# Kernel optimization log

Hardware: AMD Instinct MI355X
Metric: run time of the kernel (lower is better)

## Reference

```python
import jax, jax.numpy as jnp
import numpy as np

EMBED_DIM = 2048
NUM_HEADS = 16
HEAD_DIM = EMBED_DIM // NUM_HEADS  # 128
D_K = 128
SCALE = 1.0 / float(np.sqrt(HEAD_DIM))
LAYER_DEPTH = 6 / 12  # amrpa_layer_idx / n_amrpa_layers
BATCH, SEQ = 2, 2048


def setup_inputs() -> dict:
    key = jax.random.key(0)
    ks = jax.random.split(key, 8)
    return {
        "hidden_states": jax.random.normal(ks[0], (BATCH, SEQ, EMBED_DIM), jnp.float32),
        "c_attn_w": jax.random.normal(ks[1], (EMBED_DIM, 3 * EMBED_DIM), jnp.float32) * 0.02,
        "c_attn_b": jax.random.normal(ks[2], (3 * EMBED_DIM,), jnp.float32) * 0.02,
        "c_proj_w": jax.random.normal(ks[3], (EMBED_DIM, EMBED_DIM), jnp.float32) * 0.02,
        "c_proj_b": jax.random.normal(ks[4], (EMBED_DIM,), jnp.float32) * 0.02,
        "cam_gate": jax.random.normal(ks[5], (D_K,), jnp.float32) * 0.1,
        "cam_w0": jax.random.normal(ks[6], (1,), jnp.float32),
        "cam_w1": jax.random.normal(ks[7], (1,), jnp.float32),
    }


def reference(hidden_states, c_attn_w, c_attn_b, c_proj_w, c_proj_b, cam_gate, cam_w0, cam_w1):
    # GPT2 Conv1D-style fused QKV projection: [B,S,3E]
    qkv = hidden_states @ c_attn_w + c_attn_b
    Q, K, V = jnp.split(qkv, 3, axis=2)  # each [B,S,E]
    # NOTE: faithful to source — attention over the FULL embed dim (no head split),
    # scaled by 1/sqrt(head_dim); causal mask is computed but never applied upstream.
    attn_scores = jnp.einsum('bse,bte->bst', Q, K) * SCALE  # [B,S,S]

    # CAM: sliced low-rank channels
    Q_cam, K_cam, V_cam = Q[:, :, :D_K], K[:, :, :D_K], V[:, :, :D_K]
    # base attention map computed under no_grad in the original
    base_A = jax.lax.stop_gradient(
        jax.nn.softmax(jnp.einsum('bsd,btd->bst', Q_cam, K_cam) * SCALE, axis=-1))
    layer_weight = jax.nn.sigmoid(cam_w0[0] + cam_w1[0] * LAYER_DEPTH)
    cam_ctx = jnp.einsum('bst,btd->bsd', base_A, V_cam)            # [B,S,d_k]
    cam_bias = jnp.einsum('bsd,btd->bst', jnp.tanh(cam_ctx * cam_gate), K_cam)
    cam_bias = cam_bias * (SCALE * layer_weight)                   # cam_mask is all-ones

    final_attn = jax.nn.softmax(attn_scores + cam_bias, axis=-1)
    context = jnp.einsum('bst,bte->bse', final_attn, V)            # [B,S,E]
    output = context @ c_proj_w + c_proj_b                         # resid_dropout is identity (eval)
    return output
```

## Files before the change

### kernel.cpp

```cpp
#include <hip/hip_runtime.h>
#include <hip/hip_bf16.h>

typedef unsigned short u16;
typedef __attribute__((ext_vector_type(8))) __bf16 bf16x8;
typedef __attribute__((ext_vector_type(4))) float f32x4;
typedef __attribute__((ext_vector_type(4))) unsigned short u16x4;

#define SCALE_QK 0.08838834764831845f

__device__ __forceinline__ u16 f2bf(float x) {
  union { float f; unsigned u; } v; v.f = x;
  unsigned r = v.u + 0x7fffu + ((v.u >> 16) & 1u);
  return (u16)(r >> 16);
}

__device__ __forceinline__ void gload_lds16(const u16* g, u16* l) {
  __builtin_amdgcn_global_load_lds(
      (const __attribute__((address_space(1))) unsigned*)g,
      (__attribute__((address_space(3))) unsigned*)l, 16, 0, 0);
}

#define CFENCE() asm volatile("" ::: "memory")
#define WAITV(N) asm volatile("s_waitcnt vmcnt(" #N ")" ::: "memory")

template<bool OUT_BF16, bool HAS_BIAS, bool TWO_SEG>
__global__ __launch_bounds__(512, 2)
void g128d(const u16* __restrict__ A1, int lda1, long sA1,
           const u16* __restrict__ B1, int ldb1, long sB1, int K1,
           const u16* __restrict__ A2, int lda2, long sA2,
           const u16* __restrict__ B2, int ldb2, long sB2, int K2,
           void* __restrict__ Cv, int ldc, long sC,
           float scale, const float* __restrict__ bias, int nbx,
           int mapmode, u16* __restrict__ vTout)
{
  extern __shared__ u16 lds[];
  const int bz = blockIdx.z;
  const int nwg = gridDim.x, orig = blockIdx.x;
  const int q8 = nwg >> 3, r8 = nwg & 7;
  const int xcd = orig & 7, lp = orig >> 3;
  const int wg = (xcd < r8 ? xcd * (q8 + 1) : r8 * (q8 + 1) + (xcd - r8) * q8) + lp;
  int bx, by;
  if (mapmode == 1) {
    const int x = wg / 96, c = wg % 96;
    const int rect = c / 48, i6 = c % 48;
    by = rect * 8 + (i6 & 7);
    bx = x * 6 + (i6 >> 3);
  } else {
    by = wg / nbx; bx = wg % nbx;
  }
  const long m0 = (long)by * 256, n0 = (long)bx * 128;

  const int tid = threadIdx.x, wid = tid >> 6, lane = tid & 63;
  const int wm = wid >> 1, wn = wid & 1;
  const int rl = lane & 15, g = lane >> 4;
  const int sw = ((g ^ ((rl >> 1) & 3)) << 3);

  int aoff[4], boff[4];
#pragma unroll
  for (int i = 0; i < 4; ++i) aoff[i] = (wm * 64 + i * 16 + rl) * 32 + sw;
#pragma unroll
  for (int j = 0; j < 4; ++j) boff[j] = (wn * 64 + j * 16 + rl) * 32 + sw;

  const int srow = tid >> 2;
  const int scolX = (((tid & 3) ^ ((srow >> 1) & 3)) << 3);

  f32x4 acc[4][4];
#pragma unroll
  for (int i = 0; i < 4; ++i)
#pragma unroll
    for (int j = 0; j < 4; ++j) acc[i][j] = (f32x4){0.f, 0.f, 0.f, 0.f};

  bf16x8 avA[4], bvA[4], avB[4], bvB[4];

#define STG6(H_, OA_) {                                                  \
    const u16* sa_ = Ab + (long)srow * lda + (H_) * 32 + scolX;          \
    u16* da_ = lds + (OA_) + tid * 8;                                    \
    gload_lds16(sa_, da_);                                               \
    gload_lds16(sa_ + (long)128 * lda, da_ + 4096);                      \
    gload_lds16(Bb + (long)srow * ldb + (H_) * 32 + scolX,               \
                lds + 49152 + ((OA_) >> 1) + tid * 8); }
#define RD6(OA_, AV, BV) {                                               \
    const u16* ap_ = lds + (OA_);                                        \
    const u16* bp_ = lds + 49152 + ((OA_) >> 1);                         \
    _Pragma("unroll") for (int i_ = 0; i_ < 4; ++i_)                     \
      AV[i_] = *(const bf16x8*)(ap_ + aoff[i_]);                         \
    _Pragma("unroll") for (int j_ = 0; j_ < 4; ++j_)                     \
      BV[j_] = *(const bf16x8*)(bp_ + boff[j_]); }
#define MMCL(CAV, CBV)                                                   \
    CFENCE(); __builtin_amdgcn_s_barrier();                              \
    asm volatile("s_waitcnt lgkmcnt(0)" ::: "memory");                   \
    __builtin_amdgcn_sched_barrier(0);                                   \
    __builtin_amdgcn_s_setprio(1);                                       \
    _Pragma("unroll") for (int i_ = 0; i_ < 4; ++i_)                     \
      _Pragma("unroll") for (int j_ = 0; j_ < 4; ++j_)                   \
        acc[i_][j_] = __builtin_amdgcn_mfma_f32_16x16x32_bf16(           \
            CAV[i_], CBV[j_], acc[i_][j_], 0, 0, 0);                     \
    __builtin_amdgcn_s_setprio(0);

  const int NSEG = TWO_SEG ? 2 : 1;
#pragma unroll 1
  for (int seg = 0; seg < NSEG; ++seg) {
    const int lda = (seg == 0) ? lda1 : lda2;
    const int ldb = (seg == 0) ? ldb1 : ldb2;
    const int K   = (seg == 0) ? K1 : K2;
    const u16* Ab = ((seg == 0) ? A1 + (long)bz * sA1 : A2 + (long)bz * sA2) + m0 * (long)lda;
    const u16* Bb = ((seg == 0) ? B1 + (long)bz * sB1 : B2 + (long)bz * sB2) + n0 * (long)ldb;
    const int NT = K >> 5;

    if (NT == 4) {
      STG6(0, 0); STG6(1, 8192); STG6(2, 16384); STG6(3, 24576);
      WAITV(9);
      CFENCE(); __builtin_amdgcn_s_barrier(); CFENCE();
      RD6(0, avA, bvA);
      CFENCE();
      WAITV(6); MMCL(avA, bvA); RD6(8192,  avB, bvB); CFENCE();
      WAITV(3); MMCL(avB, bvB); RD6(16384, avA, bvA); CFENCE();
      WAITV(0); MMCL(avA, bvA); RD6(24576, avB, bvB); CFENCE();
      MMCL(avB, bvB); CFENCE();
      __builtin_amdgcn_s_barrier();
      CFENCE();
    } else {
      STG6(0, 0); STG6(1, 8192); STG6(2, 16384); STG6(3, 24576); STG6(4, 32768);
      WAITV(12);
      CFENCE(); __builtin_amdgcn_s_barrier(); CFENCE();
      RD6(0, avA, bvA);
      STG6(5, 40960);
      CFENCE();

      int rdo = 8192;
      int sto = 0;
      int hst = 6;

#pragma unroll 1
      for (int k = 0; k < NT - 6; k += 2) {
        WAITV(12);
        MMCL(avA, bvA);
        RD6(rdo, avB, bvB); rdo += 8192; if (rdo == 49152) rdo = 0;
        STG6(hst, sto); ++hst; sto += 8192; if (sto == 49152) sto = 0;
        CFENCE();
        WAITV(12);
        MMCL(avB, bvB);
        RD6(rdo, avA, bvA); rdo += 8192; if (rdo == 49152) rdo = 0;
        STG6(hst, sto); ++hst; sto += 8192; if (sto == 49152) sto = 0;
        CFENCE();
      }
      WAITV(12); MMCL(avA, bvA);
      RD6(rdo, avB, bvB); rdo += 8192; if (rdo == 49152) rdo = 0; CFENCE();
      WAITV(9);  MMCL(avB, bvB);
      RD6(rdo, avA, bvA); rdo += 8192; if (rdo == 49152) rdo = 0; CFENCE();
      WAITV(6);  MMCL(avA, bvA);
      RD6(rdo, avB, bvB); rdo += 8192; if (rdo == 49152) rdo = 0; CFENCE();
      WAITV(3);  MMCL(avB, bvB);
      RD6(rdo, avA, bvA); rdo += 8192; if (rdo == 49152) rdo = 0; CFENCE();
      WAITV(0);  MMCL(avA, bvA);
      RD6(rdo, avB, bvB); CFENCE();
      MMCL(avB, bvB); CFENCE();
      __builtin_amdgcn_s_barrier();
      CFENCE();
    }
  }
#undef STG6
#undef RD6
#undef MMCL

  const int r0 = (lane >> 4) << 2;
  const int cL = lane & 15;
#pragma unroll
  for (int i = 0; i < 4; ++i) {
#pragma unroll
    for (int j = 0; j < 4; ++j) {
      const long row = m0 + wm * 64 + i * 16 + r0;
      const long col = n0 + wn * 64 + j * 16 + cL;
      float bvs = 0.f;
      if (HAS_BIAS) bvs = bias[col];
      if (OUT_BF16) {
        u16* Cp = (u16*)Cv + (long)bz * sC;
        if (vTout && col >= 4096) {
          u16x4 t;
#pragma unroll
          for (int r = 0; r < 4; ++r) t[r] = f2bf(acc[i][j][r] * scale + bvs);
          *(u16x4*)(vTout + ((long)(row >> 11) * 2048 + (col - 4096)) * 2048 + (row & 2047)) = t;
        } else {
#pragma unroll
          for (int r = 0; r < 4; ++r)
            Cp[(row + r) * ldc + col] = f2bf(acc[i][j][r] * scale + bvs);
        }
      } else {
        float* Cp = (float*)Cv + (long)bz * sC;
#pragma unroll
        for (int r = 0; r < 4; ++r)
          Cp[(row + r) * ldc + col] = acc[i][j][r] * scale + bvs;
      }
    }
  }
}

__global__ __launch_bounds__(256)
void gemm_bt_splitk(const u16* __restrict__ A, int lda, long sA,
                    const u16* __restrict__ B, int ldb, long sB,
                    float* __restrict__ C, int ldc, long sC,
                    int Kslice, float scale)
{
  __shared__ u16 As[128 * 64];
  __shared__ u16 Bs[128 * 64];
  const int ks = blockIdx.z & 7;
  const int bz = blockIdx.z >> 3;
  const u16* Ap  = A + (long)bz * sA + ks * Kslice;
  const u16* Bp  = B + (long)bz * sB + ks * Kslice;
  const int tid  = threadIdx.x;
  const int wid  = tid >> 6;
  const int lane = tid & 63;
  const long m0  = (long)blockIdx.y * 128;
  const long n0  = (long)blockIdx.x * 128;
  const int lrow = lane >> 3;
  const int lk   = (lane & 7) << 3;
  const int wr   = wid >> 1, wc = wid & 1;

  f32x4 acc[4][4];
#pragma unroll
  for (int i = 0; i < 4; ++i)
#pragma unroll
    for (int j = 0; j < 4; ++j) acc[i][j] = (f32x4){0.f, 0.f, 0.f, 0.f};

  for (int k0 = 0; k0 < Kslice; k0 += 64) {
#pragma unroll
    for (int c4 = 0; c4 < 4; ++c4) {
      const int chunk = (wid << 2) + c4;
      gload_lds16(Ap + (m0 + (chunk << 3) + lrow) * lda + k0 + lk, &As[chunk << 9]);
      gload_lds16(Bp + (n0 + (chunk << 3) + lrow) * ldb + k0 + lk, &Bs[chunk << 9]);
    }
    __syncthreads();
#pragma unroll
    for (int kk = 0; kk < 2; ++kk) {
      bf16x8 af[4], bfr[4];
      const int kof   = (kk << 5) + ((lane >> 4) << 3);
      const int rbase = lane & 15;
#pragma unroll
      for (int i = 0; i < 4; ++i)
        af[i] = *(const bf16x8*)&As[(((wr << 6) + (i << 4) + rbase) << 6) + kof];
#pragma unroll
      for (int j = 0; j < 4; ++j)
        bfr[j] = *(const bf16x8*)&Bs[(((wc << 6) + (j << 4) + rbase) << 6) + kof];
#pragma unroll
      for (int i = 0; i < 4; ++i)
#pragma unroll
        for (int j = 0; j < 4; ++j)
          acc[i][j] = __builtin_amdgcn_mfma_f32_16x16x32_bf16(af[i], bfr[j], acc[i][j], 0, 0, 0);
    }
    __syncthreads();
  }

  const int r0 = (lane >> 4) << 2;
  const int cL = lane & 15;
  float* Cp = C + (long)bz * sC;
#pragma unroll
  for (int i = 0; i < 4; ++i) {
#pragma unroll
    for (int j = 0; j < 4; ++j) {
      const long row = m0 + (wr << 6) + (i << 4) + r0;
      const long col = n0 + (wc << 6) + (j << 4) + cL;
#pragma unroll
      for (int r = 0; r < 4; ++r)
        atomicAdd(&Cp[(row + r) * ldc + col], acc[i][j][r] * scale);
    }
  }
}

__global__ __launch_bounds__(256)
void softmax_rows2048(const float* __restrict__ src, u16* __restrict__ dst) {
  const long row = blockIdx.x;
  const float4* s = (const float4*)(src + row * 2048);
  const int tid = threadIdx.x;
  float4 a = s[tid * 2], b = s[tid * 2 + 1];
  float m = fmaxf(fmaxf(fmaxf(a.x, a.y), fmaxf(a.z, a.w)),
                  fmaxf(fmaxf(b.x, b.y), fmaxf(b.z, b.w)));
#pragma unroll
  for (int o = 32; o > 0; o >>= 1) m = fmaxf(m, __shfl_xor(m, o));
  __shared__ float redm[4];
  __shared__ float reds[4];
  if ((tid & 63) == 0) redm[tid >> 6] = m;
  __syncthreads();
  m = fmaxf(fmaxf(redm[0], redm[1]), fmaxf(redm[2], redm[3]));
  float e[8];
  e[0] = __expf(a.x - m); e[1] = __expf(a.y - m); e[2] = __expf(a.z - m); e[3] = __expf(a.w - m);
  e[4] = __expf(b.x - m); e[5] = __expf(b.y - m); e[6] = __expf(b.z - m); e[7] = __expf(b.w - m);
  float sum = e[0] + e[1] + e[2] + e[3] + e[4] + e[5] + e[6] + e[7];
#pragma unroll
  for (int o = 32; o > 0; o >>= 1) sum += __shfl_xor(sum, o);
  if ((tid & 63) == 0) reds[tid >> 6] = sum;
  __syncthreads();
  sum = reds[0] + reds[1] + reds[2] + reds[3];
  const float inv = 1.f / sum;
  u16x4 o1 = { f2bf(e[0] * inv), f2bf(e[1] * inv), f2bf(e[2] * inv), f2bf(e[3] * inv) };
  u16x4 o2 = { f2bf(e[4] * inv), f2bf(e[5] * inv), f2bf(e[6] * inv), f2bf(e[7] * inv) };
  u16x4* d = (u16x4*)(dst + row * 2048);
  d[tid * 2]     = o1;
  d[tid * 2 + 1] = o2;
}

__global__ void transpose_f32_to_bf16(const float* __restrict__ src, u16* __restrict__ dst,
                                      int R, int C) {
  __shared__ float t[32][33];
  const int c0 = blockIdx.x * 32, r0 = blockIdx.y * 32;
  const int tx = threadIdx.x, ty = threadIdx.y;
#pragma unroll
  for (int i = 0; i < 4; ++i)
    t[ty + i * 8][tx] = src[(long)(r0 + ty + i * 8) * C + c0 + tx];
  __syncthreads();
#pragma unroll
  for (int i = 0; i < 4; ++i)
    dst[(long)(c0 + ty + i * 8) * R + r0 + tx] = f2bf(t[tx][ty + i * 8]);
}

__global__ __launch_bounds__(256)
void convert_f32_to_bf16(const float* __restrict__ src, u16* __restrict__ dst, long n4) {
  long i = (long)blockIdx.x * 256 + threadIdx.x;
  if (i < n4) {
    float4 v = ((const float4*)src)[i];
    *(u16x4*)(dst + i * 4) = (u16x4){ f2bf(v.x), f2bf(v.y), f2bf(v.z), f2bf(v.w) };
  }
}

__global__ __launch_bounds__(256)
void cam_tanh_kernel(const float* __restrict__ ctx, const float* __restrict__ gate,
                     const float* __restrict__ w0, const float* __restrict__ w1,
                     u16* __restrict__ out, int n) {
  int i = blockIdx.x * 256 + threadIdx.x;
  if (i < n) {
    const float lw = 1.f / (1.f + __expf(-(w0[0] + 0.5f * w1[0])));
    int d = i & 127;
    out[i] = f2bf(tanhf(ctx[i] * gate[d]) * lw);
  }
}

__global__ __launch_bounds__(256)
void zero_f32(float* __restrict__ p, int n) {
  int i = blockIdx.x * 256 + threadIdx.x;
  if (i < n) p[i] = 0.f;
}

extern "C" void kernel_launch(void* const* d_in, const int* in_sizes, int n_in,
                              void* d_out, int out_size, void* d_ws, size_t ws_size,
                              hipStream_t stream) {
  const float* hs       = (const float*)d_in[0];
  const float* c_attn_w = (const float*)d_in[1];
  const float* c_attn_b = (const float*)d_in[2];
  const float* c_proj_w = (const float*)d_in[3];
  const float* c_proj_b = (const float*)d_in[4];
  const float* cam_gate = (const float*)d_in[5];
  const float* cam_w0   = (const float*)d_in[6];
  const float* cam_w1   = (const float*)d_in[7];
  float* out = (float*)d_out;

  char* w = (char*)d_ws;
  u16*   hs_b    = (u16*)(w + 256);
  u16*   waT_b   = (u16*)(w + 256 + 16777216UL);
  u16*   wpT_b   = (u16*)(w + 256 + 41943040UL);
  u16*   qkv_b   = (u16*)(w + 256 + 50331648UL);
  u16*   vT_b    = (u16*)(w + 256 + 100663296UL);
  float* scoresF = (float*)(w + 256 + 117440512UL);
  float* camS    = (float*)(w + 256 + 150994944UL);
  float* ctxF    = (float*)(w + 256 + 184549376UL);
  u16*   camT_b  = (u16*)(w + 256 + 186646528UL);
  u16* baseA_b = hs_b;
  u16* P_b     = (u16*)camS;
  u16* ctxE_b  = (u16*)scoresF;

  dim3 b256(256);
  const int LDSB = 147456;

  hipFuncSetAttribute((const void*)g128d<true, true, false>,
                      hipFuncAttributeMaxDynamicSharedMemorySize, LDSB);
  hipFuncSetAttribute((const void*)g128d<false, false, false>,
                      hipFuncAttributeMaxDynamicSharedMemorySize, LDSB);
  hipFuncSetAttribute((const void*)g128d<false, false, true>,
                      hipFuncAttributeMaxDynamicSharedMemorySize, LDSB);
  hipFuncSetAttribute((const void*)g128d<true, false, false>,
                      hipFuncAttributeMaxDynamicSharedMemorySize, LDSB);
  hipFuncSetAttribute((const void*)g128d<false, true, false>,
                      hipFuncAttributeMaxDynamicSharedMemorySize, LDSB);

  convert_f32_to_bf16<<<dim3(8192), b256, 0, stream>>>(hs, hs_b, 2097152L);
  transpose_f32_to_bf16<<<dim3(192, 64), dim3(32, 8), 0, stream>>>(c_attn_w, waT_b, 2048, 6144);
  transpose_f32_to_bf16<<<dim3(64, 64), dim3(32, 8), 0, stream>>>(c_proj_w, wpT_b, 2048, 2048);

  g128d<true, true, false><<<dim3(768, 1, 1), dim3(512), LDSB, stream>>>(
      hs_b, 2048, 0L, waT_b, 2048, 0L, 2048,
      nullptr, 0, 0L, nullptr, 0, 0L, 0,
      qkv_b, 6144, 0L, 1.f, c_attn_b, 48, 1, vT_b);

  g128d<false, false, false><<<dim3(128, 1, 2), dim3(512), LDSB, stream>>>(
      qkv_b, 6144, 2048L * 6144, qkv_b + 2048, 6144, 2048L * 6144, 128,
      nullptr, 0, 0L, nullptr, 0, 0L, 0,
      camS, 2048, 2048L * 2048, SCALE_QK, nullptr, 16, 0, nullptr);

  softmax_rows2048<<<dim3(4096), b256, 0, stream>>>(camS, baseA_b);

  zero_f32<<<dim3(2048), b256, 0, stream>>>(ctxF, 524288);
  gemm_bt_splitk<<<dim3(1, 16, 16), b256, 0, stream>>>(
      baseA_b, 2048, 2048L * 2048, vT_b, 2048, 2048L * 2048,
      ctxF, 128, 2048L * 128, 256, 1.f);

  cam_tanh_kernel<<<dim3(2048), b256, 0, stream>>>(ctxF, cam_gate, cam_w0, cam_w1,
                                                   camT_b, 524288);

  g128d<false, false, true><<<dim3(128, 1, 2), dim3(512), LDSB, stream>>>(
      qkv_b, 6144, 2048L * 6144, qkv_b + 2048, 6144, 2048L * 6144, 2048,
      camT_b, 128, 2048L * 128, qkv_b + 2048, 6144, 2048L * 6144, 128,
      scoresF, 2048, 2048L * 2048, SCALE_QK, nullptr, 16, 0, nullptr);

  softmax_rows2048<<<dim3(4096), b256, 0, stream>>>(scoresF, P_b);

  g128d<true, false, false><<<dim3(128, 1, 2), dim3(512), LDSB, stream>>>(
      P_b, 2048, 2048L * 2048, vT_b, 2048, 2048L * 2048, 2048,
      nullptr, 0, 0L, nullptr, 0, 0L, 0,
      ctxE_b, 2048, 2048L * 2048, 1.f, nullptr, 16, 0, nullptr);

  g128d<false, true, false><<<dim3(256, 1, 1), dim3(512), LDSB, stream>>>(
      ctxE_b, 2048, 0L, wpT_b, 2048, 0L, 2048,
      nullptr, 0, 0L, nullptr, 0, 0L, 0,
      out, 2048, 0L, 1.f, c_proj_b, 16, 0, nullptr);
}
```

Before: 345.0 us.

## Restructure GEMM main loop to K=64 tiles with triple-buffered LDS pipeline

The 256x128 GEMM kernel now stages 64-wide K tiles instead of 32-wide ones, using three 24576-element LDS buffers and an 8-way XOR swizzle. Each tile is consumed in two MFMA phases split across N halves, which shrinks the B register fragments. The old six-slot ring with hand-unrolled prologue and epilogue becomes a uniform loop with prefetch distance two. The aim is fewer barriers and waitcnts per unit of K and better LDS bank behaviour. In exchange it adds a barrier after each phase and may expose more load latency, since only two tiles are in flight.

Measured after the change: 332.1 us (median of 2 runs). 1.04x faster.

```diff
diff --git a/kernel.cpp b/kernel.cpp
--- a/kernel.cpp
+++ b/kernel.cpp
@@ -25,7 +25,7 @@
 
 template<bool OUT_BF16, bool HAS_BIAS, bool TWO_SEG>
 __global__ __launch_bounds__(512, 2)
-void g128d(const u16* __restrict__ A1, int lda1, long sA1,
+void g128q(const u16* __restrict__ A1, int lda1, long sA1,
            const u16* __restrict__ B1, int ldb1, long sB1, int K1,
            const u16* __restrict__ A2, int lda2, long sA2,
            const u16* __restrict__ B2, int ldb2, long sB2, int K2,
@@ -53,16 +53,18 @@
   const int tid = threadIdx.x, wid = tid >> 6, lane = tid & 63;
   const int wm = wid >> 1, wn = wid & 1;
   const int rl = lane & 15, g = lane >> 4;
-  const int sw = ((g ^ ((rl >> 1) & 3)) << 3);
-
-  int aoff[4], boff[4];
-#pragma unroll
-  for (int i = 0; i < 4; ++i) aoff[i] = (wm * 64 + i * 16 + rl) * 32 + sw;
-#pragma unroll
-  for (int j = 0; j < 4; ++j) boff[j] = (wn * 64 + j * 16 + rl) * 32 + sw;
-
-  const int srow = tid >> 2;
-  const int scolX = (((tid & 3) ^ ((srow >> 1) & 3)) << 3);
+  const int xa = rl & 7;
+  const int uk0 = ((g ^ xa) << 3);
+  const int uk1 = (((4 + g) ^ xa) << 3);
+
+  int aoffb[4], boffb[4];
+#pragma unroll
+  for (int i = 0; i < 4; ++i) aoffb[i] = (wm * 64 + i * 16 + rl) * 64;
+#pragma unroll
+  for (int j = 0; j < 4; ++j) boffb[j] = 16384 + (wn * 64 + j * 16 + rl) * 64;
+
+  const int ra = tid >> 3;
+  const int xcol = (((tid & 7) ^ ((tid >> 3) & 7)) << 3);
 
   f32x4 acc[4][4];
 #pragma unroll
@@ -70,32 +72,38 @@
 #pragma unroll
     for (int j = 0; j < 4; ++j) acc[i][j] = (f32x4){0.f, 0.f, 0.f, 0.f};
 
-  bf16x8 avA[4], bvA[4], avB[4], bvB[4];
-
-#define STG6(H_, OA_) {                                                  \
-    const u16* sa_ = Ab + (long)srow * lda + (H_) * 32 + scolX;          \
-    u16* da_ = lds + (OA_) + tid * 8;                                    \
-    gload_lds16(sa_, da_);                                               \
-    gload_lds16(sa_ + (long)128 * lda, da_ + 4096);                      \
-    gload_lds16(Bb + (long)srow * ldb + (H_) * 32 + scolX,               \
-                lds + 49152 + ((OA_) >> 1) + tid * 8); }
-#define RD6(OA_, AV, BV) {                                               \
-    const u16* ap_ = lds + (OA_);                                        \
-    const u16* bp_ = lds + 49152 + ((OA_) >> 1);                         \
-    _Pragma("unroll") for (int i_ = 0; i_ < 4; ++i_)                     \
-      AV[i_] = *(const bf16x8*)(ap_ + aoff[i_]);                         \
-    _Pragma("unroll") for (int j_ = 0; j_ < 4; ++j_)                     \
-      BV[j_] = *(const bf16x8*)(bp_ + boff[j_]); }
-#define MMCL(CAV, CBV)                                                   \
+  bf16x8 av[2][4], bv[2][2];
+
+#define STG(T_, BO_) { const int k0_ = (T_) << 6;                        \
+    gload_lds16(Ab + (long)(ra      ) * lda + k0_ + xcol, lds + (BO_) +         tid * 8); \
+    gload_lds16(Ab + (long)(ra +  64) * lda + k0_ + xcol, lds + (BO_) +  4096 + tid * 8); \
+    gload_lds16(Ab + (long)(ra + 128) * lda + k0_ + xcol, lds + (BO_) +  8192 + tid * 8); \
+    gload_lds16(Ab + (long)(ra + 192) * lda + k0_ + xcol, lds + (BO_) + 12288 + tid * 8); \
+    gload_lds16(Bb + (long)(ra      ) * ldb + k0_ + xcol, lds + (BO_) + 16384 + tid * 8); \
+    gload_lds16(Bb + (long)(ra +  64) * ldb + k0_ + xcol, lds + (BO_) + 20480 + tid * 8); }
+#define RD0(BO_) { const u16* p_ = lds + (BO_);                          \
+    _Pragma("unroll") for (int i_ = 0; i_ < 4; ++i_) {                   \
+      av[0][i_] = *(const bf16x8*)(p_ + aoffb[i_] + uk0);                \
+      av[1][i_] = *(const bf16x8*)(p_ + aoffb[i_] + uk1); }              \
+    _Pragma("unroll") for (int j_ = 0; j_ < 2; ++j_) {                   \
+      bv[0][j_] = *(const bf16x8*)(p_ + boffb[j_] + uk0);                \
+      bv[1][j_] = *(const bf16x8*)(p_ + boffb[j_] + uk1); } }
+#define RD1(BO_) { const u16* p_ = lds + (BO_);                          \
+    _Pragma("unroll") for (int j_ = 0; j_ < 2; ++j_) {                   \
+      bv[0][j_] = *(const bf16x8*)(p_ + boffb[2 + j_] + uk0);            \
+      bv[1][j_] = *(const bf16x8*)(p_ + boffb[2 + j_] + uk1); } }
+#define MMPH(JB_)                                                        \
     CFENCE(); __builtin_amdgcn_s_barrier();                              \
     asm volatile("s_waitcnt lgkmcnt(0)" ::: "memory");                   \
     __builtin_amdgcn_sched_barrier(0);                                   \
     __builtin_amdgcn_s_setprio(1);                                       \
-    _Pragma("unroll") for (int i_ = 0; i_ < 4; ++i_)                     \
-      _Pragma("unroll") for (int j_ = 0; j_ < 4; ++j_)                   \
-        acc[i_][j_] = __builtin_amdgcn_mfma_f32_16x16x32_bf16(           \
-            CAV[i_], CBV[j_], acc[i_][j_], 0, 0, 0);                     \
-    __builtin_amdgcn_s_setprio(0);
+    _Pragma("unroll") for (int k_ = 0; k_ < 2; ++k_)                     \
+      _Pragma("unroll") for (int i_ = 0; i_ < 4; ++i_)                   \
+        _Pragma("unroll") for (int j_ = 0; j_ < 2; ++j_)                 \
+          acc[i_][(JB_) + j_] = __builtin_amdgcn_mfma_f32_16x16x32_bf16( \
+              av[k_][i_], bv[k_][j_], acc[i_][(JB_) + j_], 0, 0, 0);     \
+    __builtin_amdgcn_s_setprio(0);                                       \
+    CFENCE(); __builtin_amdgcn_s_barrier(); CFENCE();
 
   const int NSEG = TWO_SEG ? 2 : 1;
 #pragma unroll 1
@@ -105,63 +113,33 @@
     const int K   = (seg == 0) ? K1 : K2;
     const u16* Ab = ((seg == 0) ? A1 + (long)bz * sA1 : A2 + (long)bz * sA2) + m0 * (long)lda;
     const u16* Bb = ((seg == 0) ? B1 + (long)bz * sB1 : B2 + (long)bz * sB2) + n0 * (long)ldb;
-    const int NT = K >> 5;
-
-    if (NT == 4) {
-      STG6(0, 0); STG6(1, 8192); STG6(2, 16384); STG6(3, 24576);
-      WAITV(9);
-      CFENCE(); __builtin_amdgcn_s_barrier(); CFENCE();
-      RD6(0, avA, bvA);
-      CFENCE();
-      WAITV(6); MMCL(avA, bvA); RD6(8192,  avB, bvB); CFENCE();
-      WAITV(3); MMCL(avB, bvB); RD6(16384, avA, bvA); CFENCE();
-      WAITV(0); MMCL(avA, bvA); RD6(24576, avB, bvB); CFENCE();
-      MMCL(avB, bvB); CFENCE();
-      __builtin_amdgcn_s_barrier();
-      CFENCE();
-    } else {
-      STG6(0, 0); STG6(1, 8192); STG6(2, 16384); STG6(3, 24576); STG6(4, 32768);
-      WAITV(12);
-      CFENCE(); __builtin_amdgcn_s_barrier(); CFENCE();
-      RD6(0, avA, bvA);
-      STG6(5, 40960);
-      CFENCE();
-
-      int rdo = 8192;
-      int sto = 0;
-      int hst = 6;
-
+    const int NT = K >> 6;
+
+    STG(0, 0); STG(1, 24576);
+    WAITV(6);
+    CFENCE(); __builtin_amdgcn_s_barrier(); CFENCE();
+
+    int bo = 0;
 #pragma unroll 1
-      for (int k = 0; k < NT - 6; k += 2) {
-        WAITV(12);
-        MMCL(avA, bvA);
-        RD6(rdo, avB, bvB); rdo += 8192; if (rdo == 49152) rdo = 0;
-        STG6(hst, sto); ++hst; sto += 8192; if (sto == 49152) sto = 0;
-        CFENCE();
-        WAITV(12);
-        MMCL(avB, bvB);
-        RD6(rdo, avA, bvA); rdo += 8192; if (rdo == 49152) rdo = 0;
-        STG6(hst, sto); ++hst; sto += 8192; if (sto == 49152) sto = 0;
-        CFENCE();
+    for (int t = 0; t < NT; ++t) {
+      RD0(bo);
+      if (t + 2 < NT) {
+        int bos = bo - 24576; if (bos < 0) bos = 49152;
+        STG(t + 2, bos);
+        WAITV(6);
+      } else if (t + 1 < NT) {
+        WAITV(0);
       }
-      WAITV(12); MMCL(avA, bvA);
-      RD6(rdo, avB, bvB); rdo += 8192; if (rdo == 49152) rdo = 0; CFENCE();
-      WAITV(9);  MMCL(avB, bvB);
-      RD6(rdo, avA, bvA); rdo += 8192; if (rdo == 49152) rdo = 0; CFENCE();
-      WAITV(6);  MMCL(avA, bvA);
-      RD6(rdo, avB, bvB); rdo += 8192; if (rdo == 49152) rdo = 0; CFENCE();
-      WAITV(3);  MMCL(avB, bvB);
-      RD6(rdo, avA, bvA); rdo += 8192; if (rdo == 49152) rdo = 0; CFENCE();
-      WAITV(0);  MMCL(avA, bvA);
-      RD6(rdo, avB, bvB); CFENCE();
-      MMCL(avB, bvB); CFENCE();
-      __builtin_amdgcn_s_barrier();
-      CFENCE();
+      MMPH(0)
+      RD1(bo);
+      MMPH(2)
+      bo += 24576; if (bo == 73728) bo = 0;
     }
   }
-#undef STG6
-#undef RD6
-#undef MMCL
+#undef STG
+#undef RD0
+#undef RD1
+#undef MMPH
 
   const int r0 = (lane >> 4) << 2;
   const int cL = lane & 15;
@@ -176,10 +154,10 @@
       if (OUT_BF16) {
         u16* Cp = (u16*)Cv + (long)bz * sC;
         if (vTout && col >= 4096) {
-          u16x4 t;
-#pragma unroll
-          for (int r = 0; r < 4; ++r) t[r] = f2bf(acc[i][j][r] * scale + bvs);
-          *(u16x4*)(vTout + ((long)(row >> 11) * 2048 + (col - 4096)) * 2048 + (row & 2047)) = t;
+          u16x4 tq;
+#pragma unroll
+          for (int r = 0; r < 4; ++r) tq[r] = f2bf(acc[i][j][r] * scale + bvs);
+          *(u16x4*)(vTout + ((long)(row >> 11) * 2048 + (col - 4096)) * 2048 + (row & 2047)) = tq;
         } else {
 #pragma unroll
           for (int r = 0; r < 4; ++r)
@@ -369,27 +347,27 @@
   dim3 b256(256);
   const int LDSB = 147456;
 
-  hipFuncSetAttribute((const void*)g128d<true, true, false>,
+  hipFuncSetAttribute((const void*)g128q<true, true, false>,
                       hipFuncAttributeMaxDynamicSharedMemorySize, LDSB);
-  hipFuncSetAttribute((const void*)g128d<false, false, false>,
+  hipFuncSetAttribute((const void*)g128q<false, false, false>,
                       hipFuncAttributeMaxDynamicSharedMemorySize, LDSB);
-  hipFuncSetAttribute((const void*)g128d<false, false, true>,
+  hipFuncSetAttribute((const void*)g128q<false, false, true>,
                       hipFuncAttributeMaxDynamicSharedMemorySize, LDSB);
-  hipFuncSetAttribute((const void*)g128d<true, false, false>,
+  hipFuncSetAttribute((const void*)g128q<true, false, false>,
                       hipFuncAttributeMaxDynamicSharedMemorySize, LDSB);
-  hipFuncSetAttribute((const void*)g128d<false, true, false>,
+  hipFuncSetAttribute((const void*)g128q<false, true, false>,
                       hipFuncAttributeMaxDynamicSharedMemorySize, LDSB);
 
   convert_f32_to_bf16<<<dim3(8192), b256, 0, stream>>>(hs, hs_b, 2097152L);
   transpose_f32_to_bf16<<<dim3(192, 64), dim3(32, 8), 0, stream>>>(c_attn_w, waT_b, 2048, 6144);
   transpose_f32_to_bf16<<<dim3(64, 64), dim3(32, 8), 0, stream>>>(c_proj_w, wpT_b, 2048, 2048);
 
-  g128d<true, true, false><<<dim3(768, 1, 1), dim3(512), LDSB, stream>>>(
+  g128q<true, true, false><<<dim3(768, 1, 1), dim3(512), LDSB, stream>>>(
       hs_b, 2048, 0L, waT_b, 2048, 0L, 2048,
       nullptr, 0, 0L, nullptr, 0, 0L, 0,
       qkv_b, 6144, 0L, 1.f, c_attn_b, 48, 1, vT_b);
 
-  g128d<false, false, false><<<dim3(128, 1, 2), dim3(512), LDSB, stream>>>(
+  g128q<false, false, false><<<dim3(128, 1, 2), dim3(512), LDSB, stream>>>(
       qkv_b, 6144, 2048L * 6144, qkv_b + 2048, 6144, 2048L * 6144, 128,
       nullptr, 0, 0L, nullptr, 0, 0L, 0,
       camS, 2048, 2048L * 2048, SCALE_QK, nullptr, 16, 0, nullptr);
@@ -404,19 +382,19 @@
   cam_tanh_kernel<<<dim3(2048), b256, 0, stream>>>(ctxF, cam_gate, cam_w0, cam_w1,
                                                    camT_b, 524288);
 
-  g128d<false, false, true><<<dim3(128, 1, 2), dim3(512), LDSB, stream>>>(
+  g128q<false, false, true><<<dim3(128, 1, 2), dim3(512), LDSB, stream>>>(
       qkv_b, 6144, 2048L * 6144, qkv_b + 2048, 6144, 2048L * 6144, 2048,
       camT_b, 128, 2048L * 128, qkv_b + 2048, 6144, 2048L * 6144, 128,
       scoresF, 2048, 2048L * 2048, SCALE_QK, nullptr, 16, 0, nullptr);
 
   softmax_rows2048<<<dim3(4096), b256, 0, stream>>>(scoresF, P_b);
 
-  g128d<true, false, false><<<dim3(128, 1, 2), dim3(512), LDSB, stream>>>(
+  g128q<true, false, false><<<dim3(128, 1, 2), dim3(512), LDSB, stream>>>(
       P_b, 2048, 2048L * 2048, vT_b, 2048, 2048L * 2048, 2048,
       nullptr, 0, 0L, nullptr, 0, 0L, 0,
       ctxE_b, 2048, 2048L * 2048, 1.f, nullptr, 16, 0, nullptr);
 
-  g128d<false, true, false><<<dim3(256, 1, 1), dim3(512), LDSB, stream>>>(
+  g128q<false, true, false><<<dim3(256, 1, 1), dim3(512), LDSB, stream>>>(
       ctxE_b, 2048, 0L, wpT_b, 2048, 0L, 2048,
       nullptr, 0, 0L, nullptr, 0, 0L, 0,
       out, 2048, 0L, 1.f, c_proj_b, 16, 0, nullptr);
```
